# Kernel tuning notes

Measured on AMD Instinct MI355X. Metric: run time of the kernel, lower is better.

Reference implementation:

```python
import jax, jax.numpy as jnp
import numpy as np

B, T, I, H = 4096, 28, 28, 512  # batch, timesteps, input_size, hidden_size


def setup_inputs() -> dict:
    key = jax.random.key(0)
    ks = jax.random.split(key, 32)
    def rn(k, shape, scale=0.04):
        return jax.random.normal(k, shape, dtype=jnp.float32) * scale
    inp = {"x": jax.random.normal(ks[0], (B, T, I), dtype=jnp.float32)}
    i = 1
    # PyTorch GRU params: gate order (r, z, n); layer0 input=28, layer1 input=2*H (bidirectional)
    for layer, in_dim in [(0, I), (1, 2 * H)]:
        for d in ["", "r"]:
            inp[f"W_ih_l{layer}{d}"] = rn(ks[i], (3 * H, in_dim)); i += 1
            inp[f"W_hh_l{layer}{d}"] = rn(ks[i], (3 * H, H)); i += 1
            inp[f"b_ih_l{layer}{d}"] = rn(ks[i], (3 * H,)); i += 1
            inp[f"b_hh_l{layer}{d}"] = rn(ks[i], (3 * H,)); i += 1
    inp["fc1_w"] = rn(ks[i], (256, 2 * H)); i += 1
    inp["fc1_b"] = rn(ks[i], (256,)); i += 1
    inp["bn_gamma"] = jnp.ones((256,), jnp.float32)
    inp["bn_beta"] = jnp.zeros((256,), jnp.float32)
    inp["bn_mean"] = jnp.zeros((256,), jnp.float32)
    inp["bn_var"] = jnp.ones((256,), jnp.float32)
    inp["fc2_w"] = rn(ks[i], (10, 256)); i += 1
    inp["fc2_b"] = rn(ks[i], (10,))
    return inp


def _gru_dir(x, W_ih, W_hh, b_ih, b_hh, reverse):
    # x: [B, T, I]; PyTorch GRU cell, gate order r, z, n; h0 = 0
    Bb = x.shape[0]
    Hh = W_hh.shape[1]
    gx = jnp.einsum('bti,gi->btg', x, W_ih) + b_ih  # precompute input gates [B,T,3H]
    if reverse:
        gx = gx[:, ::-1]
    def step(h, gxt):
        gh = h @ W_hh.T + b_hh
        r = jax.nn.sigmoid(gxt[:, :Hh] + gh[:, :Hh])
        z = jax.nn.sigmoid(gxt[:, Hh:2 * Hh] + gh[:, Hh:2 * Hh])
        n = jnp.tanh(gxt[:, 2 * Hh:] + r * gh[:, 2 * Hh:])
        h = (1.0 - z) * n + z * h
        return h, h
    h0 = jnp.zeros((Bb, Hh), x.dtype)
    _, hs = jax.lax.scan(step, h0, jnp.swapaxes(gx, 0, 1))
    hs = jnp.swapaxes(hs, 0, 1)  # [B,T,H]
    if reverse:
        hs = hs[:, ::-1]
    return hs


def reference(x, W_ih_l0, W_hh_l0, b_ih_l0, b_hh_l0, W_ih_l0r, W_hh_l0r, b_ih_l0r, b_hh_l0r,
              W_ih_l1, W_hh_l1, b_ih_l1, b_hh_l1, W_ih_l1r, W_hh_l1r, b_ih_l1r, b_hh_l1r,
              fc1_w, fc1_b, bn_gamma, bn_beta, bn_mean, bn_var, fc2_w, fc2_b):
    xr = x.reshape(-1, 28, 28)
    # layer 0 (bidirectional)
    h0f = _gru_dir(xr, W_ih_l0, W_hh_l0, b_ih_l0, b_hh_l0, False)
    h0b = _gru_dir(xr, W_ih_l0r, W_hh_l0r, b_ih_l0r, b_hh_l0r, True)
    y0 = jnp.concatenate([h0f, h0b], axis=-1)  # inter-layer dropout = identity (eval)
    # layer 1 (bidirectional)
    h1f = _gru_dir(y0, W_ih_l1, W_hh_l1, b_ih_l1, b_hh_l1, False)
    h1b = _gru_dir(y0, W_ih_l1r, W_hh_l1r, b_ih_l1r, b_hh_l1r, True)
    y1 = jnp.concatenate([h1f, h1b], axis=-1)
    last = y1[:, -1, :]  # [B, 1024]
    z1 = last @ fc1_w.T + fc1_b
    zbn = (z1 - bn_mean) * jax.lax.rsqrt(bn_var + 1e-5) * bn_gamma + bn_beta
    a = jax.nn.relu(zbn)  # head dropout = identity (eval)
    logits = a @ fc2_w.T + fc2_b
    return jax.nn.log_softmax(logits, axis=-1)
```

## Files before the change

### kernel.cpp

```cpp
#include <hip/hip_runtime.h>

#define DEV __device__ __forceinline__
typedef unsigned short us;
typedef __bf16 bf8 __attribute__((ext_vector_type(8)));
typedef float  f4  __attribute__((ext_vector_type(4)));

DEV us f2bf(float f){
  unsigned int u = __builtin_bit_cast(unsigned int, f);
  u = u + 0x7fffu + ((u >> 16) & 1u);
  return (us)(u >> 16);
}
DEV float bf2f(us u){ unsigned int v = ((unsigned int)u) << 16; return __builtin_bit_cast(float, v); }
DEV float sigm(float x){ return 1.f/(1.f + __expf(-x)); }
DEV bf8 ldb(const us* p){ return *reinterpret_cast<const bf8*>(p); }
DEV f4 mfma(bf8 a, bf8 b, f4 c){ return __builtin_amdgcn_mfma_f32_16x16x32_bf16(a, b, c, 0, 0, 0); }

DEV void gload16(const us* g, us* l){
  __builtin_amdgcn_global_load_lds(
    (const __attribute__((address_space(1))) unsigned int*)g,
    (__attribute__((address_space(3))) unsigned int*)l, 16, 0, 0);
}

constexpr size_t OFF_WHH0F  = 0;
constexpr size_t OFF_WHH0R  = OFF_WHH0F + 1536ull*512*2;
constexpr size_t OFF_WIH0F  = OFF_WHH0R + 1536ull*512*2;
constexpr size_t OFF_WIH0R  = OFF_WIH0F + 1536ull*32*2;
constexpr size_t OFF_WIH1   = OFF_WIH0R + 1536ull*32*2;
constexpr size_t OFF_WHH1   = OFF_WIH1  + 1536ull*1024*2;
constexpr size_t OFF_WIH1R  = OFF_WHH1  + 1536ull*512*2;
constexpr size_t OFF_FC1W   = OFF_WIH1R + 1536ull*1024*2;
constexpr size_t OFF_FC2W   = OFF_FC1W  + 256ull*1024*2;
constexpr size_t OFF_BRZ0   = OFF_FC2W  + 16ull*256*2;
constexpr size_t OFF_BNIH0  = OFF_BRZ0  + 2*1024*4;
constexpr size_t OFF_BNHH0  = OFF_BNIH0 + 2*512*4;
constexpr size_t OFF_BRZ1   = OFF_BNHH0 + 2*512*4;
constexpr size_t OFF_BNIH1  = OFF_BRZ1  + 1024*4;
constexpr size_t OFF_BNHH1  = OFF_BNIH1 + 512*4;
constexpr size_t OFF_BRZ1R  = OFF_BNHH1 + 512*4;
constexpr size_t OFF_BNIH1R = OFF_BRZ1R + 1024*4;
constexpr size_t OFF_BNHH1R = OFF_BNIH1R+ 512*4;
constexpr size_t OFF_SC2    = OFF_BNHH1R+ 512*4;
constexpr size_t OFF_SH2    = OFF_SC2   + 256*4;
constexpr size_t OFF_FC2B   = OFF_SH2   + 256*4;
constexpr size_t OFF_Y0B    = OFF_FC2B  + 64;
constexpr size_t OFF_Y0FC   = OFF_Y0B   + 4096ull*28*512*2;
constexpr size_t OFF_GX     = OFF_Y0FC  + 4096ull*4*512*2;
constexpr size_t OFF_H0BF   = OFF_GX    + 4ull*4096*1536*2;
constexpr size_t OFF_H0F32  = OFF_H0BF  + 2ull*4096*512*2;
constexpr size_t OFF_H1BF   = OFF_H0F32 + 4096ull*512*4;
constexpr size_t OFF_H1F32  = OFF_H1BF  + 2ull*4096*512*2;
constexpr size_t OFF_H1B    = OFF_H1F32 + 4096ull*512*4;
constexpr size_t OFF_XB     = OFF_H1B   + 4096ull*512*2;
constexpr size_t OFF_BAR    = OFF_XB    + 4096ull*28*32*2;

constexpr int FL_GRP  = 64;
constexpr int FL_SLOT = 16*FL_GRP;
constexpr int FL_TOTAL= 16*FL_SLOT;

constexpr long PPH   = 4096ll*512;
constexpr long PLANE = 4096ll*1536;

__global__ void prep_kernel(
  const float* __restrict__ x,
  const float* __restrict__ Wih0, const float* __restrict__ Whh0,
  const float* __restrict__ bih0, const float* __restrict__ bhh0,
  const float* __restrict__ Wih0r,const float* __restrict__ Whh0r,
  const float* __restrict__ bih0r,const float* __restrict__ bhh0r,
  const float* __restrict__ Wih1, const float* __restrict__ Whh1,
  const float* __restrict__ bih1, const float* __restrict__ bhh1,
  const float* __restrict__ Wih1r,const float* __restrict__ bih1r,
  const float* __restrict__ bhh1r,
  const float* __restrict__ fc1w, const float* __restrict__ fc1b,
  const float* __restrict__ gma,  const float* __restrict__ bta,
  const float* __restrict__ mean, const float* __restrict__ var,
  const float* __restrict__ fc2w, const float* __restrict__ fc2b,
  us* __restrict__ whh0f, us* __restrict__ whh0r,
  us* __restrict__ wih0f, us* __restrict__ wih0r,
  us* __restrict__ wih1,  us* __restrict__ whh1, us* __restrict__ wih1r,
  us* __restrict__ fc1wb, us* __restrict__ fc2wp,
  float* __restrict__ brz0, float* __restrict__ bnih0, float* __restrict__ bnhh0,
  float* __restrict__ brz1, float* __restrict__ bnih1, float* __restrict__ bnhh1,
  float* __restrict__ brz1r,float* __restrict__ bnih1r,float* __restrict__ bnhh1r,
  float* __restrict__ sc2,  float* __restrict__ sh2,   float* __restrict__ fc2bp,
  us* __restrict__ xbp, unsigned* __restrict__ flp)
{
  const int tid = blockIdx.x * blockDim.x + threadIdx.x;
  const int np  = gridDim.x * blockDim.x;
  for (int i = tid; i < 1536*512; i += np){
    whh0f[i] = f2bf(Whh0[i]);
    whh0r[i] = f2bf(Whh0r[i]);
    whh1[i]  = f2bf(Whh1[i]);
  }
  for (int i = tid; i < 1536*32; i += np){
    int n = i >> 5, k = i & 31;
    wih0f[i] = (k < 28) ? f2bf(Wih0[n*28 + k])  : (us)0;
    wih0r[i] = (k < 28) ? f2bf(Wih0r[n*28 + k]) : (us)0;
  }
  for (int i = tid; i < 1536*1024; i += np){
    wih1[i]  = f2bf(Wih1[i]);
    wih1r[i] = f2bf(Wih1r[i]);
  }
  for (int i = tid; i < 256*1024; i += np) fc1wb[i] = f2bf(fc1w[i]);
  for (int i = tid; i < 16*256;   i += np){
    int n = i / 256; fc2wp[i] = (n < 10) ? f2bf(fc2w[i]) : (us)0;
  }
  for (int i = tid; i < 4096*28; i += np){
    const float* src = x + (size_t)i * 28;
    us* dst = xbp + (size_t)i * 32;
    #pragma unroll
    for (int k = 0; k < 28; ++k) dst[k] = f2bf(src[k]);
    dst[28] = dst[29] = dst[30] = dst[31] = 0;
  }
  for (int i = tid; i < FL_TOTAL; i += np) flp[i] = 0;
  for (int i = tid; i < 1024; i += np){
    brz0[i]        = bih0[i]  + bhh0[i];
    brz0[1024 + i] = bih0r[i] + bhh0r[i];
    brz1[i]        = bih1[i]  + bhh1[i];
    brz1r[i]       = bih1r[i] + bhh1r[i];
  }
  for (int i = tid; i < 512; i += np){
    bnih0[i]       = bih0[1024 + i];   bnhh0[i]       = bhh0[1024 + i];
    bnih0[512 + i] = bih0r[1024 + i];  bnhh0[512 + i] = bhh0r[1024 + i];
    bnih1[i]       = bih1[1024 + i];   bnhh1[i]       = bhh1[1024 + i];
    bnih1r[i]      = bih1r[1024 + i];  bnhh1r[i]      = bhh1r[1024 + i];
  }
  for (int i = tid; i < 256; i += np){
    float s = gma[i] * rsqrtf(var[i] + 1e-5f);
    sc2[i] = s;
    sh2[i] = (fc1b[i] - mean[i]) * s + bta[i];
  }
  for (int i = tid; i < 16; i += np) fc2bp[i] = (i < 10) ? fc2b[i] : 0.f;
}

__global__ __launch_bounds__(256) void gemm_kernel(
  const us* __restrict__ s0, long s0m, long s0t, int K0,
  const us* __restrict__ s1, long s1m, long s1t,
  const us* __restrict__ B, int Kw, int nk, int tshift, int nMtiles,
  us* __restrict__ C, long cT)
{
  __shared__ __align__(16) us As[2*128*32];
  __shared__ __align__(16) us Bs[2*128*32];

  const int tid = threadIdx.x, bid = blockIdx.x;
  const int mtile = bid % nMtiles, ntile = bid / nMtiles;
  const int Mbase = mtile * 128, Nbase = ntile * 128;
  const int mask = (1 << tshift) - 1;
  const int ktSplit = K0 >> 5;

  const int w = tid >> 6, lane = tid & 63, ln = lane & 15, lq = lane >> 4;
  const int wm = w >> 1, wn = w & 1;

  const int r0 = tid >> 2, g0 = tid & 3;
  const int R0 = Mbase + r0, R1 = R0 + 64;
  const int m0 = R0 >> tshift, sl0 = R0 & mask;
  const int m1 = R1 >> tshift, sl1 = R1 & mask;
  const us* pA00 = s0 + (size_t)m0*s0m + (long)sl0*s0t + g0*8;
  const us* pA01 = s1 + (size_t)m0*s1m + (long)sl0*s1t + g0*8;
  const us* pA10 = s0 + (size_t)m1*s0m + (long)sl1*s0t + g0*8;
  const us* pA11 = s1 + (size_t)m1*s1m + (long)sl1*s1t + g0*8;
  const us* pB0  = B + (size_t)(Nbase + r0     )*Kw + g0*8;
  const us* pB1  = B + (size_t)(Nbase + r0 + 64)*Kw + g0*8;

  auto stage = [&](int buf, int kt){
    const int kc = kt*32;
    const us* a0; const us* a1;
    if (kt < ktSplit){ a0 = pA00 + kc; a1 = pA10 + kc; }
    else             { a0 = pA01 + (kc - K0); a1 = pA11 + (kc - K0); }
    gload16(a0,       &As[buf +        w*512]);
    gload16(a1,       &As[buf + 2048 + w*512]);
    gload16(pB0 + kc, &Bs[buf +        w*512]);
    gload16(pB1 + kc, &Bs[buf + 2048 + w*512]);
  };

  stage(0, 0);
  __syncthreads();

  f4 acc[4][4] = {};

  for (int kt = 0; kt < nk; ++kt){
    const int buf = (kt & 1) * 4096;
    const bool more = (kt + 1) < nk;
    if (more) stage(buf ^ 4096, kt + 1);
    bf8 a0 = ldb(&As[buf + (wm*64 +  0 + ln)*32 + lq*8]);
    bf8 a1 = ldb(&As[buf + (wm*64 + 16 + ln)*32 + lq*8]);
    bf8 a2 = ldb(&As[buf + (wm*64 + 32 + ln)*32 + lq*8]);
    bf8 a3 = ldb(&As[buf + (wm*64 + 48 + ln)*32 + lq*8]);
    bf8 b0 = ldb(&Bs[buf + (wn*64 +  0 + ln)*32 + lq*8]);
    bf8 b1 = ldb(&Bs[buf + (wn*64 + 16 + ln)*32 + lq*8]);
    bf8 b2 = ldb(&Bs[buf + (wn*64 + 32 + ln)*32 + lq*8]);
    bf8 b3 = ldb(&Bs[buf + (wn*64 + 48 + ln)*32 + lq*8]);
    acc[0][0] = mfma(a0, b0, acc[0][0]); acc[0][1] = mfma(a0, b1, acc[0][1]);
    acc[0][2] = mfma(a0, b2, acc[0][2]); acc[0][3] = mfma(a0, b3, acc[0][3]);
    acc[1][0] = mfma(a1, b0, acc[1][0]); acc[1][1] = mfma(a1, b1, acc[1][1]);
    acc[1][2] = mfma(a1, b2, acc[1][2]); acc[1][3] = mfma(a1, b3, acc[1][3]);
    acc[2][0] = mfma(a2, b0, acc[2][0]); acc[2][1] = mfma(a2, b1, acc[2][1]);
    acc[2][2] = mfma(a2, b2, acc[2][2]); acc[2][3] = mfma(a2, b3, acc[2][3]);
    acc[3][0] = mfma(a3, b0, acc[3][0]); acc[3][1] = mfma(a3, b1, acc[3][1]);
    acc[3][2] = mfma(a3, b2, acc[3][2]); acc[3][3] = mfma(a3, b3, acc[3][3]);
    if (more) __syncthreads();
  }

  #pragma unroll
  for (int mtf = 0; mtf < 4; ++mtf){
    #pragma unroll
    for (int ntf = 0; ntf < 4; ++ntf){
      const int col = Nbase + wn*64 + ntf*16 + ln;
      #pragma unroll
      for (int e = 0; e < 4; ++e){
        const int R = Mbase + wm*64 + mtf*16 + lq*4 + e;
        const int m = R >> tshift, sl = R & mask;
        C[(size_t)sl*cT + (size_t)m*1536 + col] = f2bf(acc[mtf][ntf][e]);
      }
    }
  }
}

template<int USE_X>
__global__ __launch_bounds__(512) void gru_coop_kernel(
  const us* __restrict__ W, const us* __restrict__ Wx,
  const us* __restrict__ xb, const us* __restrict__ gxAll,
  us* __restrict__ hPP, float* __restrict__ hF,
  us* __restrict__ y, long ymstride, int ymode,
  const float* __restrict__ brz, const float* __restrict__ bni,
  const float* __restrict__ bnh,
  int s0, int nsteps, int rev, unsigned* __restrict__ flags)
{
  __shared__ us Ws[96*520];
  __shared__ us Wxs[96*40];
  __shared__ us As[2*256*40];

  const int tid = threadIdx.x, bid = blockIdx.x;
  const int hcb = bid >> 4, nm = bid & 15;
  const size_t Mbase = (size_t)nm * 256;
  const int hcBase = hcb * 32;
  const int w = tid >> 6, lane = tid & 63, ln = lane & 15, lq = lane >> 4;
  unsigned* const fl = flags + nm * FL_GRP;

  #pragma unroll
  for (int i = 0; i < 12; ++i){
    const int q = tid + i*512;
    const int rl = q >> 6, seg = q & 63;
    const int grow = (rl >> 5)*512 + hcBase + (rl & 31);
    *reinterpret_cast<uint4*>(&Ws[rl*520 + seg*8]) =
      *reinterpret_cast<const uint4*>(&W[(size_t)grow*512 + seg*8]);
  }
  if (USE_X && tid < 384){
    const int rl = tid >> 2, seg = tid & 3;
    const int grow = (rl >> 5)*512 + hcBase + (rl & 31);
    *reinterpret_cast<uint4*>(&Wxs[rl*40 + seg*8]) =
      *reinterpret_cast<const uint4*>(&Wx[(size_t)grow*32 + seg*8]);
  }

  auto stA = [&](int buf, int q, uint4 v){
    const int row = q >> 2, grp = q & 3;
    *reinterpret_cast<uint4*>(&As[buf + row*40 + grp*8]) = v;
  };

  float hreg[2][2][4];
  #pragma unroll
  for (int nt = 0; nt < 2; ++nt)
    #pragma unroll
    for (int mt = 0; mt < 2; ++mt)
      #pragma unroll
      for (int e = 0; e < 4; ++e) hreg[nt][mt][e] = 0.f;
  if (s0 > 0){
    #pragma unroll
    for (int nt = 0; nt < 2; ++nt){
      const int ch = hcBase + nt*16 + ln;
      #pragma unroll
      for (int mt = 0; mt < 2; ++mt)
        #pragma unroll
        for (int e = 0; e < 4; ++e){
          const size_t m = Mbase + w*32 + mt*16 + lq*4 + e;
          hreg[nt][mt][e] = hF[m*512 + ch];
        }
    }
  }

  for (int s = s0; s < s0 + nsteps; ++s){
    const int t = rev ? 27 - s : s;
    const bool first = (s == 0);
    const bool last  = (s == s0 + nsteps - 1);

    const us* hin; long hinm;
    us* hOut = nullptr;
    if (ymode == 1){ hin = y + (size_t)(rev ? t + 1 : t - 1) * 512; hinm = ymstride; }
    else if (ymode == 2){ hin = y + (size_t)((s - 1) & 3) * 512; hinm = ymstride; }
    else {
      hin  = hPP + (size_t)(s & 1) * PPH; hinm = 512;
      hOut = hPP + (size_t)((s & 1) ^ 1) * PPH;
    }

    auto ldH = [&](int kt, int q) -> uint4 {
      const int row = q >> 2, grp = q & 3;
      return *reinterpret_cast<const uint4*>(&hin[(Mbase + row)*hinm + kt*32 + grp*8]);
    };

    f4 acc[3][2][2] = {};
    f4 accNX[2][2] = {};

    us gxv[12][4];
    if (!USE_X){
      const us* gx = gxAll + (size_t)(s - s0) * PLANE;
      #pragma unroll
      for (int nt = 0; nt < 2; ++nt){
        const int ch = hcBase + nt*16 + ln;
        #pragma unroll
        for (int mt = 0; mt < 2; ++mt){
          #pragma unroll
          for (int e = 0; e < 4; ++e){
            const size_t m = Mbase + w*32 + mt*16 + lq*4 + e;
            const us* gxr = gx + m*1536;
            gxv[0 + nt*2 + mt][e] = gxr[ch];
            gxv[4 + nt*2 + mt][e] = gxr[512 + ch];
            gxv[8 + nt*2 + mt][e] = gxr[1024 + ch];
          }
        }
      }
    }

    if (USE_X){
      #pragma unroll
      for (int i = 0; i < 2; ++i){
        const int q = tid + i*512;
        const int row = q >> 2, grp = q & 3;
        uint4 v = *reinterpret_cast<const uint4*>(
          &xb[((Mbase + row)*28 + (size_t)t)*32 + grp*8]);
        stA(0, q, v);
      }
    }
    uint4 s1a{}, s1b{}, s2a{}, s2b{};
    const int B0 = USE_X ? 10240 : 0;
    if (!first){
      stA(B0, tid, ldH(0, tid)); stA(B0, tid + 512, ldH(0, tid + 512));
      s1a = ldH(1, tid); s1b = ldH(1, tid + 512);
      s2a = ldH(2, tid); s2b = ldH(2, tid + 512);
    }
    __syncthreads();

    if (USE_X){
      bf8 a0 = ldb(&As[(w*32 +  0 + ln)*40 + lq*8]);
      bf8 a1 = ldb(&As[(w*32 + 16 + ln)*40 + lq*8]);
      #pragma unroll
      for (int g = 0; g < 3; ++g){
        #pragma unroll
        for (int nt = 0; nt < 2; ++nt){
          bf8 b = ldb(&Wxs[(g*32 + nt*16 + ln)*40 + lq*8]);
          if (g == 2){
            accNX[nt][0] = mfma(a0, b, accNX[nt][0]);
            accNX[nt][1] = mfma(a1, b, accNX[nt][1]);
          } else {
            acc[g][nt][0] = mfma(a0, b, acc[g][nt][0]);
            acc[g][nt][1] = mfma(a1, b, acc[g][nt][1]);
          }
        }
      }
      if (!first) __syncthreads();
    }

    if (!first){
      for (int kt = 0; kt < 16; ++kt){
        const int buf = B0 ^ ((kt & 1) * 10240);
        bf8 a0 = ldb(&As[buf + (w*32 +  0 + ln)*40 + lq*8]);
        bf8 a1 = ldb(&As[buf + (w*32 + 16 + ln)*40 + lq*8]);
        const int kc = kt*32 + lq*8;
        #pragma unroll
        for (int g = 0; g < 3; ++g){
          #pragma unroll
          for (int nt = 0; nt < 2; ++nt){
            bf8 b = ldb(&Ws[(g*32 + nt*16 + ln)*520 + kc]);
            acc[g][nt][0] = mfma(a0, b, acc[g][nt][0]);
            acc[g][nt][1] = mfma(a1, b, acc[g][nt][1]);
          }
        }
        if (kt < 15){
          stA(buf ^ 10240, tid, s1a); stA(buf ^ 10240, tid + 512, s1b);
          s1a = s2a; s1b = s2b;
          if (kt + 3 < 16){ s2a = ldH(kt + 3, tid); s2b = ldH(kt + 3, tid + 512); }
          __syncthreads();
        }
      }
    }

    #pragma unroll
    for (int nt = 0; nt < 2; ++nt){
      const int ch = hcBase + nt*16 + ln;
      const float br = brz[ch], bz = brz[512 + ch], bi = bni[ch], bh = bnh[ch];
      #pragma unroll
      for (int mt = 0; mt < 2; ++mt){
        #pragma unroll
        for (int e = 0; e < 4; ++e){
          const size_t m = Mbase + w*32 + mt*16 + lq*4 + e;
          float rr = acc[0][nt][mt][e] + br;
          float zz = acc[1][nt][mt][e] + bz;
          float xr = accNX[nt][mt][e];
          if (!USE_X){
            rr += bf2f(gxv[0 + nt*2 + mt][e]);
            zz += bf2f(gxv[4 + nt*2 + mt][e]);
            xr += bf2f(gxv[8 + nt*2 + mt][e]);
          }
          float r = sigm(rr);
          float z = sigm(zz);
          float n = tanhf(xr + bi + r*(acc[2][nt][mt][e] + bh));
          float hprev = first ? 0.f : hreg[nt][mt][e];
          float h = (1.f - z)*n + z*hprev;
          hreg[nt][mt][e] = h;
          if (last && hF) hF[m*512 + ch] = h;
          us hb = f2bf(h);
          if (ymode == 0)      hOut[m*512 + ch] = hb;
          else if (ymode == 1) y[m*ymstride + (size_t)t*512 + ch] = hb;
          else                 y[m*ymstride + (size_t)(s - s0)*512 + ch] = hb;
        }
      }
    }

    if (!last){
      __syncthreads();
      if (tid < 16){
        if (tid == 0)
          __hip_atomic_store(fl + hcb, (unsigned)(s + 1),
                             __ATOMIC_RELAXED, __HIP_MEMORY_SCOPE_AGENT);
        const unsigned tgt = (unsigned)(s + 1);
        int guard = 0;
        while (__hip_atomic_load(fl + tid, __ATOMIC_RELAXED,
                                 __HIP_MEMORY_SCOPE_AGENT) < tgt){
          __builtin_amdgcn_s_sleep(1);
          if (++guard > (1 << 18)) break;
        }
      }
      __syncthreads();
    }
  }
}

__global__ void gate1b_kernel(
  const us* __restrict__ gxb, const float* __restrict__ brz,
  const float* __restrict__ bni, const float* __restrict__ bnh,
  us* __restrict__ h1b)
{
  const int i = blockIdx.x * blockDim.x + threadIdx.x;
  if (i >= 4096*512) return;
  const int m = i >> 9, ch = i & 511;
  const us* g = gxb + (size_t)m*1536;
  float r = sigm(bf2f(g[ch]) + brz[ch]);
  float z = sigm(bf2f(g[512 + ch]) + brz[512 + ch]);
  float n = tanhf(bf2f(g[1024 + ch]) + bni[ch] + r*bnh[ch]);
  h1b[i] = f2bf((1.f - z)*n);
}

__global__ __launch_bounds__(512) void head_kernel(
  const us* __restrict__ h1f, const us* __restrict__ h1b,
  const us* __restrict__ fc1w, const us* __restrict__ fc2wp,
  const float* __restrict__ sc2, const float* __restrict__ sh2,
  const float* __restrict__ fc2b, float* __restrict__ out)
{
  constexpr int APS = 1048;
  __shared__ us As[32 * APS];
  __shared__ us actS[32 * 264];
  __shared__ float lg[32 * 16];
  const int tid = threadIdx.x;
  const size_t row0 = (size_t)blockIdx.x * 32;
  const int w = tid >> 6, lane = tid & 63, ln = lane & 15, lq = lane >> 4;

  for (int i = tid; i < 32*128; i += 512){
    int r = i >> 7, g = i & 127, col = g*8;
    uint4 v = (col < 512)
      ? *reinterpret_cast<const uint4*>(h1f + (row0 + r)*512 + col)
      : *reinterpret_cast<const uint4*>(h1b + (row0 + r)*512 + (col - 512));
    *reinterpret_cast<uint4*>(&As[r*APS + col]) = v;
  }
  __syncthreads();

  {
    f4 acc[2][2] = {};
    for (int kt = 0; kt < 32; ++kt){
      const int kc = kt*32 + lq*8;
      bf8 a0 = ldb(&As[ln*APS + kc]);
      bf8 a1 = ldb(&As[(16 + ln)*APS + kc]);
      #pragma unroll
      for (int nt = 0; nt < 2; ++nt){
        const int col = w*32 + nt*16 + ln;
        bf8 b = ldb(&fc1w[(size_t)col*1024 + kc]);
        acc[0][nt] = mfma(a0, b, acc[0][nt]);
        acc[1][nt] = mfma(a1, b, acc[1][nt]);
      }
    }
    #pragma unroll
    for (int nt = 0; nt < 2; ++nt){
      const int col = w*32 + nt*16 + ln;
      const float sc = sc2[col], sh = sh2[col];
      #pragma unroll
      for (int mt = 0; mt < 2; ++mt)
        #pragma unroll
        for (int e = 0; e < 4; ++e){
          float v = fmaxf(acc[mt][nt][e]*sc + sh, 0.f);
          actS[(mt*16 + lq*4 + e)*264 + col] = f2bf(v);
        }
    }
    __syncthreads();
  }

  if (w == 0){
    f4 acc[2] = {};
    for (int kt = 0; kt < 8; ++kt){
      const int kc = kt*32 + lq*8;
      bf8 a0 = ldb(&actS[ln*264 + kc]);
      bf8 a1 = ldb(&actS[(16 + ln)*264 + kc]);
      bf8 b  = ldb(&fc2wp[ln*256 + kc]);
      acc[0] = mfma(a0, b, acc[0]);
      acc[1] = mfma(a1, b, acc[1]);
    }
    const float bb = fc2b[ln];
    #pragma unroll
    for (int mt = 0; mt < 2; ++mt)
      #pragma unroll
      for (int e = 0; e < 4; ++e)
        lg[(mt*16 + lq*4 + e)*16 + ln] = acc[mt][e] + bb;
  }
  __syncthreads();
  if (tid < 32){
    const int r = tid;
    float mx = -1e30f;
    for (int cc = 0; cc < 10; ++cc) mx = fmaxf(mx, lg[r*16 + cc]);
    float sum = 0.f;
    for (int cc = 0; cc < 10; ++cc) sum += __expf(lg[r*16 + cc] - mx);
    const float lse = mx + logf(sum);
    for (int cc = 0; cc < 10; ++cc)
      out[(row0 + r)*10 + cc] = lg[r*16 + cc] - lse;
  }
}

extern "C" void kernel_launch(void* const* d_in, const int* in_sizes, int n_in,
                              void* d_out, int out_size, void* d_ws, size_t ws_size,
                              hipStream_t stream)
{
  (void)in_sizes; (void)n_in; (void)out_size; (void)ws_size;
  char* ws = (char*)d_ws;
  auto US = [&](size_t off){ return (us*)(ws + off); };
  auto FP = [&](size_t off){ return (float*)(ws + off); };

  const float* x      = (const float*)d_in[0];
  const float* Wih0   = (const float*)d_in[1];
  const float* Whh0   = (const float*)d_in[2];
  const float* bih0   = (const float*)d_in[3];
  const float* bhh0   = (const float*)d_in[4];
  const float* Wih0r  = (const float*)d_in[5];
  const float* Whh0r  = (const float*)d_in[6];
  const float* bih0r  = (const float*)d_in[7];
  const float* bhh0r  = (const float*)d_in[8];
  const float* Wih1   = (const float*)d_in[9];
  const float* Whh1   = (const float*)d_in[10];
  const float* bih1   = (const float*)d_in[11];
  const float* bhh1   = (const float*)d_in[12];
  const float* Wih1r  = (const float*)d_in[13];
  const float* bih1r  = (const float*)d_in[15];
  const float* bhh1r  = (const float*)d_in[16];
  const float* fc1w   = (const float*)d_in[17];
  const float* fc1b   = (const float*)d_in[18];
  const float* gma    = (const float*)d_in[19];
  const float* bta    = (const float*)d_in[20];
  const float* mean   = (const float*)d_in[21];
  const float* var    = (const float*)d_in[22];
  const float* fc2w   = (const float*)d_in[23];
  const float* fc2b   = (const float*)d_in[24];

  prep_kernel<<<512, 256, 0, stream>>>(
    x, Wih0, Whh0, bih0, bhh0, Wih0r, Whh0r, bih0r, bhh0r,
    Wih1, Whh1, bih1, bhh1, Wih1r, bih1r, bhh1r,
    fc1w, fc1b, gma, bta, mean, var, fc2w, fc2b,
    US(OFF_WHH0F), US(OFF_WHH0R), US(OFF_WIH0F), US(OFF_WIH0R),
    US(OFF_WIH1), US(OFF_WHH1), US(OFF_WIH1R), US(OFF_FC1W), US(OFF_FC2W),
    FP(OFF_BRZ0), FP(OFF_BNIH0), FP(OFF_BNHH0),
    FP(OFF_BRZ1), FP(OFF_BNIH1), FP(OFF_BNHH1),
    FP(OFF_BRZ1R), FP(OFF_BNIH1R), FP(OFF_BNHH1R),
    FP(OFF_SC2), FP(OFF_SH2), FP(OFF_FC2B),
    US(OFF_XB), (unsigned*)(ws + OFF_BAR));

  us* y0b  = US(OFF_Y0B);
  us* y0fc = US(OFF_Y0FC);
  us* gx   = US(OFF_GX);
  us* h1bf = US(OFF_H1BF);
  us* xb   = US(OFF_XB);
  unsigned* fl = (unsigned*)(ws + OFF_BAR);

  gru_coop_kernel<1><<<256, 512, 0, stream>>>(
    US(OFF_WHH0R), US(OFF_WIH0R), xb, nullptr,
    nullptr, nullptr, y0b, 28ll*512, 1,
    FP(OFF_BRZ0) + 1024, FP(OFF_BNIH0) + 512, FP(OFF_BNHH0) + 512,
    0, 28, 1, fl + 0*FL_SLOT);

  for (int c = 0; c < 7; ++c){
    const int t0 = 4*c;
    gru_coop_kernel<1><<<256, 512, 0, stream>>>(
      US(OFF_WHH0F), US(OFF_WIH0F), xb, nullptr,
      nullptr, FP(OFF_H0F32), y0fc, 4ll*512, 2,
      FP(OFF_BRZ0), FP(OFF_BNIH0), FP(OFF_BNHH0),
      t0, 4, 0, fl + 1*FL_SLOT);
    gemm_kernel<<<128*12, 256, 0, stream>>>(
      y0fc, 4ll*512, 512, 512,
      y0b + t0*512, 28ll*512, 512,
      US(OFF_WIH1), 1024, 32, 2, 128, gx, PLANE);
    gru_coop_kernel<0><<<256, 512, 0, stream>>>(
      US(OFF_WHH1), nullptr, nullptr, gx,
      h1bf, FP(OFF_H1F32), nullptr, 0, 0,
      FP(OFF_BRZ1), FP(OFF_BNIH1), FP(OFF_BNHH1),
      t0, 4, 0, fl + 2*FL_SLOT);
  }

  gemm_kernel<<<32*12, 256, 0, stream>>>(
    y0fc + 3*512, 4ll*512, 0, 512,
    y0b + 27*512, 28ll*512, 0,
    US(OFF_WIH1R), 1024, 32, 0, 32, gx, 0);
  gate1b_kernel<<<8192, 256, 0, stream>>>(
    gx, FP(OFF_BRZ1R), FP(OFF_BNIH1R), FP(OFF_BNHH1R), US(OFF_H1B));

  head_kernel<<<128, 512, 0, stream>>>(
    h1bf, US(OFF_H1B), US(OFF_FC1W), US(OFF_FC2W),
    FP(OFF_SC2), FP(OFF_SH2), FP(OFF_FC2B), (float*)d_out);
}
```

Baseline: 1.751 ms.

## Load GRU hidden-state MFMA operands directly from global into registers, dropping LDS staging

The recurrent GEMM no longer stages the hidden-state and x tiles through a double-buffered LDS array with a __syncthreads per k-step. Each wave now loads its own MFMA A-fragments straight from global memory into registers with a three-deep prefetch, and the k-loop is fully unrolled. This removes the LDS store/load traffic and the 16 barriers per timestep. In exchange, global loads are less coalesced (16-byte pieces strided by row), register pressure rises from the unrolled prefetch, and only one barrier after the weight load remains.

```diff
diff --git a/kernel.cpp b/kernel.cpp
--- a/kernel.cpp
+++ b/kernel.cpp
@@ -227,7 +227,6 @@
 {
   __shared__ us Ws[96*520];
   __shared__ us Wxs[96*40];
-  __shared__ us As[2*256*40];
 
   const int tid = threadIdx.x, bid = blockIdx.x;
   const int hcb = bid >> 4, nm = bid & 15;
@@ -250,11 +249,7 @@
     *reinterpret_cast<uint4*>(&Wxs[rl*40 + seg*8]) =
       *reinterpret_cast<const uint4*>(&Wx[(size_t)grow*32 + seg*8]);
   }
-
-  auto stA = [&](int buf, int q, uint4 v){
-    const int row = q >> 2, grp = q & 3;
-    *reinterpret_cast<uint4*>(&As[buf + row*40 + grp*8]) = v;
-  };
+  __syncthreads();
 
   float hreg[2][2][4];
   #pragma unroll
@@ -290,11 +285,6 @@
       hin  = hPP + (size_t)(s & 1) * PPH; hinm = 512;
       hOut = hPP + (size_t)((s & 1) ^ 1) * PPH;
     }
-
-    auto ldH = [&](int kt, int q) -> uint4 {
-      const int row = q >> 2, grp = q & 3;
-      return *reinterpret_cast<const uint4*>(&hin[(Mbase + row)*hinm + kt*32 + grp*8]);
-    };
 
     f4 acc[3][2][2] = {};
     f4 accNX[2][2] = {};
@@ -320,49 +310,36 @@
     }
 
     if (USE_X){
-      #pragma unroll
-      for (int i = 0; i < 2; ++i){
-        const int q = tid + i*512;
-        const int row = q >> 2, grp = q & 3;
-        uint4 v = *reinterpret_cast<const uint4*>(
-          &xb[((Mbase + row)*28 + (size_t)t)*32 + grp*8]);
-        stA(0, q, v);
-      }
-    }
-    uint4 s1a{}, s1b{}, s2a{}, s2b{};
-    const int B0 = USE_X ? 10240 : 0;
-    if (!first){
-      stA(B0, tid, ldH(0, tid)); stA(B0, tid + 512, ldH(0, tid + 512));
-      s1a = ldH(1, tid); s1b = ldH(1, tid + 512);
-      s2a = ldH(2, tid); s2b = ldH(2, tid + 512);
-    }
-    __syncthreads();
-
-    if (USE_X){
-      bf8 a0 = ldb(&As[(w*32 +  0 + ln)*40 + lq*8]);
-      bf8 a1 = ldb(&As[(w*32 + 16 + ln)*40 + lq*8]);
+      bf8 ax0 = ldb(&xb[((Mbase + w*32 +  0 + ln)*28 + (size_t)t)*32 + lq*8]);
+      bf8 ax1 = ldb(&xb[((Mbase + w*32 + 16 + ln)*28 + (size_t)t)*32 + lq*8]);
       #pragma unroll
       for (int g = 0; g < 3; ++g){
         #pragma unroll
         for (int nt = 0; nt < 2; ++nt){
           bf8 b = ldb(&Wxs[(g*32 + nt*16 + ln)*40 + lq*8]);
           if (g == 2){
-            accNX[nt][0] = mfma(a0, b, accNX[nt][0]);
-            accNX[nt][1] = mfma(a1, b, accNX[nt][1]);
+            accNX[nt][0] = mfma(ax0, b, accNX[nt][0]);
+            accNX[nt][1] = mfma(ax1, b, accNX[nt][1]);
           } else {
-            acc[g][nt][0] = mfma(a0, b, acc[g][nt][0]);
-            acc[g][nt][1] = mfma(a1, b, acc[g][nt][1]);
+            acc[g][nt][0] = mfma(ax0, b, acc[g][nt][0]);
+            acc[g][nt][1] = mfma(ax1, b, acc[g][nt][1]);
           }
         }
       }
-      if (!first) __syncthreads();
     }
 
     if (!first){
+      auto ldA = [&](int kt, int r16) -> bf8 {
+        return ldb(&hin[(Mbase + w*32 + r16 + ln)*hinm + kt*32 + lq*8]);
+      };
+      bf8 f0a = ldA(0, 0), f0b = ldA(0, 16);
+      bf8 f1a = ldA(1, 0), f1b = ldA(1, 16);
+      bf8 f2a = ldA(2, 0), f2b = ldA(2, 16);
+      #pragma unroll
       for (int kt = 0; kt < 16; ++kt){
-        const int buf = B0 ^ ((kt & 1) * 10240);
-        bf8 a0 = ldb(&As[buf + (w*32 +  0 + ln)*40 + lq*8]);
-        bf8 a1 = ldb(&As[buf + (w*32 + 16 + ln)*40 + lq*8]);
+        bf8 a0 = f0a, a1 = f0b;
+        f0a = f1a; f0b = f1b; f1a = f2a; f1b = f2b;
+        if (kt + 3 < 16){ f2a = ldA(kt + 3, 0); f2b = ldA(kt + 3, 16); }
         const int kc = kt*32 + lq*8;
         #pragma unroll
         for (int g = 0; g < 3; ++g){
@@ -372,12 +349,6 @@
             acc[g][nt][0] = mfma(a0, b, acc[g][nt][0]);
             acc[g][nt][1] = mfma(a1, b, acc[g][nt][1]);
           }
-        }
-        if (kt < 15){
-          stA(buf ^ 10240, tid, s1a); stA(buf ^ 10240, tid + 512, s1b);
-          s1a = s2a; s1b = s2b;
-          if (kt + 3 < 16){ s2a = ldH(kt + 3, tid); s2b = ldH(kt + 3, tid + 512); }
-          __syncthreads();
         }
       }
     }
```

Measured after the change: 1.835 ms. 4.8% more time.
